# Kernel tuning notes

Measured on AMD Instinct MI355X. Metric: run time of the kernel, lower is better.

Reference implementation:

```python
import jax, jax.numpy as jnp
import numpy as np

B, S, W, T = 16, 32, 32, 64
H2 = 512   # num_hidden*2: decoder state / encoder state size
Hf = 256   # vocab_nn hidden (= num_hidden)
F = 128    # vectorizer.vector_size
A = 128    # attn_hidden (= num_hidden // 2)
V = 32000  # vocab size; distribution over V+1 (last slot = OOV / -1 index)


def setup_inputs() -> dict:
    key = jax.random.key(0)
    ks = jax.random.split(key, 24)
    p = lambda k, shp, s=0.05: (jax.random.normal(k, shp) * s).astype(jnp.float32)
    d = {}
    d["text_states"] = p(ks[0], (B, S, W, H2), 0.5)
    d["sentence_states"] = p(ks[1], (B, S, H2), 0.5)
    d["text_length"] = jnp.clip(jax.random.randint(ks[2], (B, S), 0, W), 1, W)
    d["state"] = p(ks[3], (B, 2, H2), 0.5)
    d["summary"] = jax.random.randint(ks[4], (B, T), 0, V)
    d["summary_length"] = jnp.clip(jax.random.randint(ks[5], (B,), 0, T), 2, T)
    d["emb"] = p(ks[6], (V + 1, F), 0.02)            # vectorizer embedding
    d["W_cc"] = p(ks[7], (F + H2, F)); d["b_cc"] = jnp.zeros((F,), jnp.float32)
    d["Wx"] = p(ks[8], (F, 4 * H2)); d["Wh"] = p(ks[9], (H2, 4 * H2))
    d["b_lstm"] = jnp.zeros((4 * H2,), jnp.float32)
    d["W_a"] = p(ks[10], (2 * H2 + 1, A)); d["b_a"] = jnp.zeros((A,), jnp.float32)
    d["v_a"] = p(ks[11], (A,))
    d["W_rc"] = p(ks[12], (2 * H2, H2)); d["b_rc"] = jnp.zeros((H2,), jnp.float32)
    d["W1"] = p(ks[13], (2 * H2, Hf)); d["b1"] = jnp.zeros((Hf,), jnp.float32)
    d["W2"] = p(ks[14], (Hf, V + 1)); d["b2"] = jnp.zeros((V + 1,), jnp.float32)
    return d


def reference(text_states, sentence_states, text_length, state, summary,
              summary_length, emb, W_cc, b_cc, Wx, Wh, b_lstm,
              W_a, b_a, v_a, W_rc, b_rc, W1, b1, W2, b2):
    SW = S * W
    ws = text_states.reshape(B, SW, H2)  # word states, flattened source positions
    ss = jnp.broadcast_to(sentence_states[:, :, None, :], (B, S, W, H2)).reshape(B, SW, H2)
    cat_states = jnp.concatenate([ws, ss], -1)               # (B,SW,4H)
    mask = (jnp.arange(W) < text_length[:, :, None]).reshape(B, SW)
    Wa_word, Wa_out, wa_cov = W_a[:H2], W_a[H2:2 * H2], W_a[2 * H2]
    ws_a = ws @ Wa_word + b_a                                # step-invariant, (B,SW,A)

    def step(carry, xs):
        st, coverage, ctx, loss = carry
        tok_t, tok_tp1, t = xs
        valid = ((summary_length - t - 1) > 0).astype(jnp.float32)
        # CombineContext + LSTM decoder cell
        x = jnp.concatenate([emb[tok_t], ctx], 1) @ W_cc + b_cc
        h, c = st[:, 0], st[:, 1]
        gi, gf, gg, go = jnp.split(x @ Wx + h @ Wh + b_lstm, 4, axis=1)
        c_new = jax.nn.sigmoid(gf) * c + jax.nn.sigmoid(gi) * jnp.tanh(gg)
        out = jax.nn.sigmoid(go) * jnp.tanh(c_new)           # (B,2H)
        # hierarchical attention with coverage feature (input dim 4H+1)
        scores = jnp.tanh(ws_a + (out @ Wa_out)[:, None, :]
                          + coverage[:, :, None] * wa_cov) @ v_a
        attn = jax.nn.softmax(jnp.where(mask, scores, -1e9), axis=1)
        ctx4 = jnp.einsum('bn,bnd->bd', attn, cat_states)    # (B,4H)
        ctx_new = ctx4 @ W_rc + b_rc                         # ReduceContextVector -> (B,2H)
        # vocabulary distribution
        hid = jax.nn.relu(jnp.concatenate([ctx_new, out], 1) @ W1 + b1)
        vocab = jax.nn.softmax(hid @ W2 + b2, axis=1)        # (B,V+1)
        tgt = jnp.where(tok_tp1 == -1, V, tok_tp1)           # map_input_indices_
        logp = jnp.log(jnp.take_along_axis(vocab, tgt[:, None], 1)[:, 0])
        covloss = jnp.minimum(coverage, attn).sum(1)
        loss = loss + valid * (-logp + covloss)              # gamma = 1
        # scatter-back semantics of timestep_wrapper: invalid rows zeroed
        attn_m = attn * valid[:, None]
        st_new = jnp.stack([out, c_new], 1) * valid[:, None, None]
        return (st_new, coverage + attn_m, ctx_new * valid[:, None], loss), None

    coverage0 = jnp.zeros((B, SW), jnp.float32)
    ctx0 = jnp.zeros((B, H2), jnp.float32)
    loss0 = jnp.zeros((B,), jnp.float32)
    xs = (summary[:, :-1].T, summary[:, 1:].T, jnp.arange(T - 1))
    (_, _, _, loss), _ = jax.lax.scan(step, (state, coverage0, ctx0, loss0), xs)
    return loss / (summary_length.astype(jnp.float32) - 1.0)
```

## Files before the change

### kernel.cpp

```cpp
#include <hip/hip_runtime.h>
#include <math.h>

#define B 16
#define S 32
#define T 64
#define H2 512
#define Hf 256
#define F 128
#define A 128
#define V 32000
#define SW 1024
#define NSTEP 63
#define VP1 32001
#define NBLK 256

__device__ __forceinline__ float frcp(float x){ return __builtin_amdgcn_rcpf(x); }
__device__ __forceinline__ float fsigm(float x){ return frcp(1.f + __expf(-x)); }
__device__ __forceinline__ float ftanh_(float x){
    float e = __expf(-2.f*fabsf(x));
    float t = (1.f - e)*frcp(1.f + e);
    return x >= 0.f ? t : -t;
}
__device__ __forceinline__ void ast(float* p, float v){
    __hip_atomic_store(p, v, __ATOMIC_RELAXED, __HIP_MEMORY_SCOPE_AGENT);
// ... 118 lines not shown
    }
}

__global__ __launch_bounds__(128) void k_wrcc(
    const float* __restrict__ W_rc, const float* __restrict__ W_cc, float* __restrict__ WRCC)
{
    __shared__ float wr[512];
    int d = blockIdx.x, f = threadIdx.x;
    for (int i = f; i < 512; i += 128) wr[i] = W_rc[(size_t)d*H2 + i];
    __syncthreads();
    float a = 0.f;
    for (int c = 0; c < H2; ++c) a += wr[c]*W_cc[(size_t)(F+c)*F + f];
    WRCC[(size_t)d*F + f] = a;
}

__global__ __launch_bounds__(128) void k_embx(
    const int* __restrict__ summary, const float* __restrict__ emb,
    const float* __restrict__ W_cc, const float* __restrict__ b_cc,
    float* __restrict__ embx)
{
    __shared__ float er[128];
    int t = blockIdx.x, b = blockIdx.y, f = threadIdx.x;
    int tok = summary[b*T + t];
    er[f] = emb[(size_t)tok*F + f];
    __syncthreads();
    float a = b_cc[f];
    for (int k = 0; k < F; ++k) a += er[k]*W_cc[(size_t)k*F + f];
    embx[((size_t)t*B + b)*F + f] = a;
}

__global__ __launch_bounds__(1024) void k_packw2(
    const float* __restrict__ W2, unsigned* __restrict__ W2h)
{
    size_t idx = (size_t)blockIdx.x*1024 + threadIdx.x;
    int rp = (int)(idx >> 15), v = (int)(idx & 32767);
    float lo = (v < VP1) ? W2[(size_t)(2*rp)*VP1 + v] : 0.f;
    float hi = (v < VP1) ? W2[(size_t)(2*rp+1)*VP1 + v] : 0.f;
    W2h[idx] = bfr(lo) | (bfr(hi) << 16);
}
__global__ __launch_bounds__(1024) void k_packws(
    const float* __restrict__ ws, unsigned* __restrict__ wsh)
{
    size_t idx = (size_t)blockIdx.x*1024 + threadIdx.x;
    int b = (int)(idx >> 18), r = (int)(idx & 262143);
    int np = r >> 9, d = r & 511;
    float lo = ws[((size_t)b*SW + 2*np)*H2 + d];
    float hi = ws[((size_t)b*SW + 2*np+1)*H2 + d];
    wsh[idx] = bfr(lo) | (bfr(hi) << 16);
}
__global__ __launch_bounds__(1024) void k_packwsa(
    const float* __restrict__ ws_aT, unsigned* __restrict__ ws_aTh)
{
    size_t idx = (size_t)blockIdx.x*1024 + threadIdx.x;
    int b = (int)(idx >> 16), r = (int)(idx & 65535);
    int ap = r >> 10, n = r & 1023;
    float lo = ws_aT[((size_t)b*A + 2*ap)*SW + n];
    float hi = ws_aT[((size_t)b*A + 2*ap+1)*SW + n];
    ws_aTh[idx] = bfr(lo) | (bfr(hi) << 16);
}
__global__ __launch_bounds__(1024) void k_packwg(
    const float* __restrict__ Wx, const float* __restrict__ Wh,
    unsigned* __restrict__ wgh)
{
    size_t idx = (size_t)blockIdx.x*1024 + threadIdx.x;
    int kp = (int)(idx >> 11), cg = (int)(idx & 2047);
    int k0 = 2*kp, k1 = 2*kp + 1;
    float lo = (k0 < F) ? Wx[(size_t)k0*2048 + cg] : Wh[(size_t)(k0-F)*2048 + cg];
    float hi = (k1 < F) ? Wx[(size_t)k1*2048 + cg] : Wh[(size_t)(k1-F)*2048 + cg];
    wgh[idx] = bfr(lo) | (bfr(hi) << 16);
}

__global__ __launch_bounds__(512, 2) void k_persist(
    const float* __restrict__ ss,
    const int* __restrict__ text_length, const int* __restrict__ summary,
    const int* __restrict__ sumlen, const float* __restrict__ state,
    const unsigned* __restrict__ wgh, const float* __restrict__ b_lstm,
    const float* __restrict__ W_a, const float* __restrict__ v_a,
    const float* __restrict__ W1, const float* __restrict__ b2,
    const unsigned* __restrict__ W2h, const unsigned* __restrict__ wsh,
    const unsigned* __restrict__ ws_aTh,
    const float* __restrict__ Wf, const float* __restrict__ bf,
    const float* __restrict__ WRCC, const float* __restrict__ bconst,
    const float* __restrict__ embx,
    float* xR, float* outR, float* hidR, float* scoresR, float* c4R,
    unsigned* wopartH, float* mpartR, float* spartR, float* m2R, float* s2R,
    float* tgtlogR, float* covlpR, float* d_out, unsigned* cnt)
{
    __shared__ unsigned W2L[16384];
    __shared__ unsigned wsaL[4096];
    __shared__ float BIG[15552];
    __shared__ float redS[576];
    __shared__ float red2[528];
    __shared__ float wo_l[128];
    __shared__ float wac_l[128], vas_l[128], b2_l[128];
    __shared__ float score_l[64], cov_l[64];
    __shared__ float c_l[128];
    __shared__ float gsum[528];
    __shared__ float asum_l[32];
    __shared__ float mred[136], sred[136], msc2[16];
    __shared__ float loss_l[16];
    __shared__ float misc[4];
    __shared__ int tl_l[32], sumlen_l[16], tgt_l[16];

    const int blk = blockIdx.x, tid = threadIdx.x;
    const int b_role = blk >> 4, sl = blk & 15;
    unsigned* arr = cnt;
    unsigned* rel = cnt + 8192;

    const int vl = tid & 127, rq = tid >> 7;
    const int dl = tid & 31, nq = tid >> 5;
    const int n3 = tid & 63, aq = tid >> 6;
    const int cc = tid & 31, kg = tid >> 5;

    unsigned wsr[32];
    #pragma unroll
    for (int j = 0; j < 32; ++j)
        wsr[j] = wsh[((size_t)b_role*512 + nq*32 + j)*512 + sl*32 + dl];
    unsigned wgr[20];
    if (blk < 64){
        const int CGg = (cc >> 3)*512 + blk*8 + (cc & 7);
        #pragma unroll
        for (int j = 0; j < 20; ++j)
            wgr[j] = wgh[(size_t)(kg*20 + j)*2048 + CGg];
    }
    #pragma unroll
    for (int q = 0; q < 32; ++q){
        int i = q*512 + tid;
        W2L[i] = W2h[(size_t)(i >> 7)*32768 + blk*128 + (i & 127)];
    }
    #pragma unroll
    for (int q = 0; q < 8; ++q){
        int i = q*512 + tid;
        wsaL[i] = ws_aTh[((size_t)(b_role*64 + (i >> 6)))*1024 + sl*64 + (i & 63)];
    }

    if (tid < 128){
        wac_l[tid] = W_a[(size_t)(2*H2)*A + tid];
        vas_l[tid] = v_a[tid];
        int v2 = blk*128 + tid;
        b2_l[tid] = (v2 < VP1) ? b2[v2] : 0.f;
    }
    if (tid < 32) tl_l[tid] = text_length[b_role*S + tid];
    if (tid < 16){ sumlen_l[tid] = sumlen[tid]; loss_l[tid] = 0.f; }
    if (tid < 64) cov_l[tid] = 0.f;
    if (blk < 64 && tid < 128){
        int b = tid >> 3, c = tid & 7;
        c_l[tid] = state[(size_t)b*2*H2 + H2 + blk*8 + c];
    }
    __syncthreads();

    unsigned gen = 0;
    for (int t = 0; t <= NSTEP; ++t){
        if (t >= 1){
            if (tid < 16) mred[tid] = mpartR[(size_t)(t-1)*256 + b_role*16 + tid];
            if (tid >= 16 && tid < 32) mred[tid] = spartR[(size_t)(t-1)*256 + b_role*16 + (tid-16)];
            __syncthreads();
            if (tid == 0){
                float M = -1e30f;
                for (int i = 0; i < 16; ++i) M = fmaxf(M, mred[i]);
                float Sv = 0.f;
                for (int i = 0; i < 16; ++i) Sv += mred[16+i]*__expf(mred[i]-M);
                misc[0] = M; misc[1] = frcp(Sv);
            }
            __syncthreads();
            if (tid < 64){
                float at = __expf(score_l[tid]-misc[0])*misc[1];
                float clp = fminf(cov_l[tid], at);
                float vm1 = (sumlen_l[b_role] - t > 0) ? 1.f : 0.f;
                cov_l[tid] += at*vm1;
                sred[tid] = clp;
            }
            __syncthreads();
            if (tid == 0){
                float s = 0.f;
                for (int i = 0; i < 64; ++i) s += sred[i];
                ast(&covlpR[(size_t)(t-1)*256 + b_role*16 + sl], s);
            }
            __syncthreads();
        }
        if (t < NSTEP && blk < 64){
            float* xh = BIG;
            float* outloc = BIG + 14336;
            float* waL = BIG + 14464;
            {
                int i2 = tid*2;
                waL[i2]   = W_a[(size_t)(H2 + blk*8 + (i2 >> 7))*A + (i2 & 127)];
                waL[i2+1] = W_a[(size_t)(H2 + blk*8 + ((i2+1) >> 7))*A + ((i2+1) & 127)];
            }
            const float* xb0 = xR + (size_t)t*B*F;
            const float* hb0 = outR + (size_t)(t > 0 ? t-1 : 0)*B*H2;
            #pragma unroll
            for (int q = 0; q < 20; ++q){
                int i = q*512 + tid;
                int b = i/640, k = i - b*640;
                float v;
                if (k < F) v = xb0[b*F + k];
                else if (t == 0) v = state[(size_t)b*2*H2 + (k - F)];
                else v = hb0[b*H2 + (k - F)] * ((sumlen_l[b] - t > 0) ? 1.f : 0.f);
                xh[i] = v;
            }
            __syncthreads();
            for (int b = 0; b < 16; ++b){
                const float* xb = &BIG[b*640 + kg*40];
                float s0 = 0.f, s1 = 0.f;
                #pragma unroll
                for (int j = 0; j < 20; ++j){
                    unsigned wu = wgr[j];
                    s0 = fmaf(xb[2*j],   blo(wu), s0);
                    s1 = fmaf(xb[2*j+1], bhi(wu), s1);
                }
                float p = s0 + s1;
                p += __shfl_xor(p, 32);
                if ((kg & 1) == 0)
                    BIG[10240 + (b*8 + (kg >> 1))*32 + cc] = p;
            }
            __syncthreads();
            {
                int b = tid >> 5, c2 = tid & 31;
                float s = 0.f;
                #pragma unroll
                for (int q = 0; q < 8; ++q) s += BIG[10240 + (b*8 + q)*32 + c2];
                gsum[b*33 + c2] = s;
            }
            __syncthreads();
            if (tid < 128){
                int b = tid >> 3, c = tid & 7, col = blk*8 + c;
                float gi = gsum[b*33 + c]      + b_lstm[col];
                float gf = gsum[b*33 + 8 + c]  + b_lstm[H2 + col];
                float gg = gsum[b*33 + 16 + c] + b_lstm[2*H2 + col];
                float go = gsum[b*33 + 24 + c] + b_lstm[3*H2 + col];
                float cold = c_l[tid];
                float cn = fsigm(gf)*cold + fsigm(gi)*ftanh_(gg);
                float o = fsigm(go)*ftanh_(cn);
                float valid = (sumlen_l[b] - t - 1 > 0) ? 1.f : 0.f;
                c_l[tid] = cn*valid;
                outloc[tid] = o;
                ast(&outR[(size_t)t*B*H2 + b*H2 + col], o);
            }
            __syncthreads();
            {
                int o2 = tid*2;
                int b = o2 >> 6, ap0 = o2 & 63;
                #pragma unroll
                for (int w = 0; w < 2; ++w){
                    int ap = ap0 + w, a0 = ap*2;
                    float acc0 = 0.f, acc1 = 0.f;
                    #pragma unroll
                    for (int j = 0; j < 8; ++j){
                        float ov = outloc[b*8 + j];
                        acc0 = fmaf(ov, waL[j*128 + a0],     acc0);
                        acc1 = fmaf(ov, waL[j*128 + a0 + 1], acc1);
                    }
                    astu(&wopartH[(size_t)t*65536 + blk*1024 + b*64 + ap],
                         bfr(acc0) | (bfr(acc1) << 16));
                }
            }
        }
        gen++; gbar(arr, rel, gen);

        if (t < NSTEP){
            {
                int ap = tid & 63, grp = tid >> 6;
                const unsigned* wp = wopartH + (size_t)t*65536 + (size_t)(grp*8)*1024
                                     + b_role*64 + ap;
                float lo = 0.f, hi = 0.f;
                #pragma unroll
                for (int q = 0; q < 8; ++q){
                    unsigned u = wp[(size_t)q*1024];
                    lo += blo(u); hi += bhi(u);
                }
                red2[ap*8 + grp] = lo;
                redS[ap*8 + grp] = hi;
            }
            __syncthreads();
            if (tid < 64){
                float lo = 0.f, hi = 0.f;
                #pragma unroll
                for (int q = 0; q < 8; ++q){ lo += red2[tid*8+q]; hi += redS[tid*8+q]; }
                wo_l[tid*2] = lo; wo_l[tid*2+1] = hi;
            }
            __syncthreads();
            {
                float cv = cov_l[n3];
                float acc = 0.f;
                #pragma unroll
                for (int i = 0; i < 8; ++i){
                    unsigned u = wsaL[(aq*8 + i)*64 + n3];
                    int a0 = aq*16 + 2*i;
                    acc = fmaf(ftanh_(blo(u) + wo_l[a0] + cv*wac_l[a0]), vas_l[a0], acc);
                    acc = fmaf(ftanh_(bhi(u) + wo_l[a0+1] + cv*wac_l[a0+1]), vas_l[a0+1], acc);
                }
                redS[aq*72 + n3] = acc;
            }
            __syncthreads();
            if (tid < 64){
                float s = 0.f;
                #pragma unroll
                for (int q = 0; q < 8; ++q) s += redS[q*72 + tid];
                int nn = sl*64 + tid;
                float sc = ((nn & 31) < tl_l[nn >> 5]) ? s : -1e9f;
                score_l[tid] = sc;
                ast(&scoresR[(size_t)t*B*SW + b_role*SW + nn], sc);
            }
            __syncthreads();
            if (tid == 0){
                float m = score_l[0];
                for (int i = 1; i < 64; ++i) m = fmaxf(m, score_l[i]);
                float s = 0.f;
                for (int i = 0; i < 64; ++i) s += __expf(score_l[i]-m);
                ast(&mpartR[(size_t)t*256 + b_role*16 + sl], m);
                ast(&spartR[(size_t)t*256 + b_role*16 + sl], s);
            }
        }
        gen++; gbar(arr, rel, gen);

        {
            float* SC = BIG;
            float* AT = BIG + 1024;
            float* redc = BIG + 2048;
            float* hidL = BIG + 2560;
            float* parts = BIG + 6784;
            float* logitl = BIG;
            if (t < NSTEP){
                #pragma unroll
                for (int q = 0; q < 2; ++q)
                    SC[q*512 + tid] = scoresR[(size_t)t*B*SW + b_role*SW + q*512 + tid];
                if (tid < 16) mred[tid] = mpartR[(size_t)t*256 + b_role*16 + tid];
                if (tid >= 16 && tid < 32) mred[tid] = spartR[(size_t)t*256 + b_role*16 + (tid-16)];
            }
            if (t >= 1){
                if (tid < 16){ int tok = summary[tid*T + t]; tgt_l[tid] = (tok == -1) ? V : tok; }
                #pragma unroll
                for (int q = 0; q < 8; ++q){
                    int idx = q*512 + tid;
                    int r = idx >> 4, b = idx & 15;
                    hidL[b*264 + r] = hidR[(size_t)(t-1)*B*Hf + idx];
                }
            }
            __syncthreads();
            if (t < NSTEP){
                if (tid == 0){
                    float M = -1e30f;
                    for (int i = 0; i < 16; ++i) M = fmaxf(M, mred[i]);
                    float Sv = 0.f;
                    for (int i = 0; i < 16; ++i) Sv += mred[16+i]*__expf(mred[i]-M);
                    misc[0] = M; misc[1] = frcp(Sv);
                }
            }
            __syncthreads();
            if (t < NSTEP){
                #pragma unroll
                for (int q = 0; q < 2; ++q){
                    int n = q*512 + tid;
                    AT[n] = __expf(SC[n]-misc[0])*misc[1];
                }
            }
            __syncthreads();
            if (t < NSTEP){
                if (tid < 32){
                    float s = 0.f;
                    #pragma unroll
                    for (int j = 0; j < 32; ++j) s += AT[tid*32 + ((j + tid) & 31)];
                    asum_l[tid] = s;
                }
                float acc0 = 0.f, acc1 = 0.f;
                const float2* at2 = (const float2*)&AT[nq*64];
                #pragma unroll
                for (int j = 0; j < 32; ++j){
                    unsigned u = wsr[j];
                    float2 av = at2[j];
                    acc0 = fmaf(av.x, blo(u), acc0);
                    acc1 = fmaf(av.y, bhi(u), acc1);
                }
                redc[nq*32 + dl] = acc0 + acc1;
            }
            if (t >= 1){
                unsigned wreg[32];
                #pragma unroll
                for (int i = 0; i < 32; ++i) wreg[i] = W2L[(rq*32 + i)*128 + vl];
                for (int b = 0; b < 16; ++b){
                    const float2* hb2 = (const float2*)&hidL[b*264 + rq*64];
                    float a0 = 0.f, a1 = 0.f;
                    #pragma unroll
                    for (int i = 0; i < 32; ++i){
                        unsigned u = wreg[i];
                        float2 h = hb2[i];
                        a0 = fmaf(h.x, blo(u), a0);
                        a1 = fmaf(h.y, bhi(u), a1);
                    }
                    parts[rq*2176 + vl*17 + b] = a0 + a1;
                }
            }
            __syncthreads();
            if (t < NSTEP){
                if (tid < 32){
                    float s = 0.f;
                    #pragma unroll
                    for (int q = 0; q < 16; ++q) s += redc[q*32 + tid];
                    ast(&c4R[(size_t)t*B*SW + b_role*SW + sl*32 + tid], s);
                } else if (tid < 64){
                    int d2 = tid - 32;
                    float s = 0.f;
                    const float* ssb = ss + ((size_t)(b_role*S))*H2 + sl*32 + d2;
                    #pragma unroll 4
                    for (int s2 = 0; s2 < 32; ++s2)
                        s = fmaf(asum_l[s2], ssb[(size_t)s2*H2], s);
                    ast(&c4R[(size_t)t*B*SW + b_role*SW + 512 + sl*32 + d2], s);
                }
            }
            __syncthreads();
            if (t >= 1){
                #pragma unroll
                for (int j = 0; j < 4; ++j){
                    int idx = tid*4 + j;
                    int vl2 = idx >> 4, bb = idx & 15;
                    float s = parts[0*2176 + vl2*17 + bb]
                            + parts[1*2176 + vl2*17 + bb]
                            + parts[2*2176 + vl2*17 + bb]
                            + parts[3*2176 + vl2*17 + bb];
                    int v2 = blk*128 + vl2;
                    float lg = (v2 < VP1) ? (s + b2_l[vl2]) : -1e30f;
                    if (v2 < VP1 && v2 == tgt_l[bb])
                        ast(&tgtlogR[(size_t)(t-1)*16 + bb], lg);
                    logitl[vl2*17 + bb] = lg;
                }
                __syncthreads();
                if (tid < 128){
                    int b2i = tid & 15, grp = tid >> 4;
                    float m = -1e30f;
                    #pragma unroll
                    for (int i = 0; i < 16; ++i) m = fmaxf(m, logitl[(grp*16+i)*17 + b2i]);
                    mred[grp*17 + b2i] = m;
                }
                __syncthreads();
                if (tid < 16){
                    float m = -1e30f;
                    #pragma unroll
                    for (int q = 0; q < 8; ++q) m = fmaxf(m, mred[q*17 + tid]);
                    msc2[tid] = m;
                }
                __syncthreads();
                if (tid < 128){
                    int b2i = tid & 15, grp = tid >> 4;
                    float Mb = msc2[b2i];
                    float s = 0.f;
                    #pragma unroll
                    for (int i = 0; i < 16; ++i) s += __expf(logitl[(grp*16+i)*17 + b2i] - Mb);
                    sred[grp*17 + b2i] = s;
                }
                __syncthreads();
                if (tid < 16){
                    float s = 0.f;
                    #pragma unroll
                    for (int q = 0; q < 8; ++q) s += sred[q*17 + tid];
                    ast(&m2R[(size_t)(t-1)*B*256 + tid*256 + blk], msc2[tid]);
                    ast(&s2R[(size_t)(t-1)*B*256 + tid*256 + blk], s);
                }
            }
        }
        gen++; gbar(arr, rel, gen);

        if (t < NSTEP && sl < 12){
            float* c4l = BIG;
            float* OL  = BIG + 1024;
            float* redd = BIG + 1536;
            #pragma unroll
            for (int q = 0; q < 2; ++q)
                c4l[q*512 + tid] = c4R[(size_t)t*B*SW + b_role*SW + q*512 + tid];
            if (tid < 512) OL[tid] = outR[(size_t)t*B*H2 + b_role*H2 + tid];
            __syncthreads();
            int cl = tid & 31, kq = tid >> 5;
            if (sl < 8){
                int col = sl*32 + cl;
                float acc = 0.f;
                const float* wp = Wf + (size_t)(kq*64)*Hf + col;
                #pragma unroll 4
                for (int i = 0; i < 64; ++i)
                    acc = fmaf(c4l[kq*64+i], wp[(size_t)i*Hf], acc);
                const float* w1p = W1 + (size_t)(H2 + kq*32)*Hf + col;
                #pragma unroll 4
                for (int i = 0; i < 32; ++i)
                    acc = fmaf(OL[kq*32+i], w1p[(size_t)i*Hf], acc);
                redd[kq*32 + cl] = acc;
                __syncthreads();
                if (tid < 32){
                    float z = 0.f;
                    #pragma unroll
                    for (int q = 0; q < 16; ++q) z += redd[q*32 + tid];
                    z += bf[sl*32 + tid];
                    ast(&hidR[(size_t)t*B*Hf + (sl*32 + tid)*16 + b_role], fmaxf(z, 0.f));
                }
            } else {
                int f = (sl-8)*32 + cl;
                float acc = 0.f;
                const float* wp = WRCC + (size_t)(kq*64)*F + f;
                #pragma unroll 4
                for (int i = 0; i < 64; ++i)
                    acc = fmaf(c4l[kq*64+i], wp[(size_t)i*F], acc);
                redd[kq*32 + cl] = acc;
                __syncthreads();
                if (tid < 32){
                    int f2 = (sl-8)*32 + tid;
                    float z = 0.f;
                    #pragma unroll
                    for (int q = 0; q < 16; ++q) z += redd[q*32 + tid];
                    float vld = (sumlen_l[b_role] - t - 1 > 0) ? 1.f : 0.f;
                    float xv = embx[((size_t)(t+1)*B + b_role)*F + f2] + vld*(z + bconst[f2]);
                    ast(&xR[(size_t)(t+1)*B*F + b_role*F + f2], xv);
                }
            }
        }
        if (t >= 1 && blk == 255 && tid < 256){
            int tf = t - 1;
            int bb = tid >> 4, g = tid & 15;
            float mv[16];
            float m = -1e30f;
            #pragma unroll
            for (int j = 0; j < 16; ++j){
                mv[j] = m2R[(size_t)tf*B*256 + bb*256 + g + j*16];
                m = fmaxf(m, mv[j]);
            }
            #pragma unroll
            for (int off = 1; off < 16; off <<= 1) m = fmaxf(m, __shfl_xor(m, off, 16));
            float s = 0.f;
            #pragma unroll
            for (int j = 0; j < 16; ++j)
                s += s2R[(size_t)tf*B*256 + bb*256 + g + j*16]*__expf(mv[j]-m);
            #pragma unroll
            for (int off = 1; off < 16; off <<= 1) s += __shfl_xor(s, off, 16);
            if (g == 0){
                float cl = 0.f;
                for (int q = 0; q < 16; ++q) cl += covlpR[(size_t)tf*256 + bb*16 + q];
                float tlg = tgtlogR[(size_t)tf*16 + bb];
                float logp = tlg - m - __logf(s);
                float vld = (sumlen_l[bb] - tf - 1 > 0) ? 1.f : 0.f;
                loss_l[bb] += vld*(-logp + cl);
                if (t == NSTEP) d_out[bb] = loss_l[bb] / ((float)sumlen_l[bb] - 1.f);
            }
        }
        if (t == NSTEP) break;
        gen++; gbar(arr, rel, gen);
    }
}

extern "C" void kernel_launch(void* const* d_in, const int* in_sizes, int n_in,
                              void* d_out, int out_size, void* d_ws, size_t ws_size,
                              hipStream_t stream) {
    const float* text_states = (const float*)d_in[0];
    const float* sent_states = (const float*)d_in[1];
    const int*   text_length = (const int*)d_in[2];
    const float* state       = (const float*)d_in[3];
    const int*   summary     = (const int*)d_in[4];
    const int*   sumlen      = (const int*)d_in[5];
    const float* emb    = (const float*)d_in[6];
    const float* W_cc   = (const float*)d_in[7];
    const float* b_cc   = (const float*)d_in[8];
    const float* Wx     = (const float*)d_in[9];
    const float* Wh     = (const float*)d_in[10];
    const float* b_lstm = (const float*)d_in[11];
    const float* W_a    = (const float*)d_in[12];
    const float* b_a    = (const float*)d_in[13];
    const float* v_a    = (const float*)d_in[14];
    const float* W_rc   = (const float*)d_in[15];
    const float* b_rc   = (const float*)d_in[16];
    const float* W1     = (const float*)d_in[17];
    const float* b1     = (const float*)d_in[18];
    const float* W2     = (const float*)d_in[19];
    const float* b2     = (const float*)d_in[20];
    float* out = (float*)d_out;

    float* p = (float*)d_ws;
    float* ws_aT   = p; p += (size_t)B*A*SW;
    float* Wf      = p; p += (size_t)1024*Hf;
    float* bfv     = p; p += Hf;
    float* WRCC    = p; p += (size_t)1024*F;
    float* bconst  = p; p += F;
    float* embx    = p; p += (size_t)T*B*F;
    float* xR      = p; p += (size_t)(NSTEP+1)*B*F;
    float* outR    = p; p += (size_t)(NSTEP+1)*B*H2;
    float* hidR    = p; p += (size_t)(NSTEP+1)*B*Hf;
    float* scoresR = p; p += (size_t)(NSTEP+1)*B*SW;
    float* c4R     = p; p += (size_t)(NSTEP+1)*B*SW;
    float* mpartR  = p; p += (size_t)(NSTEP+1)*256;
    float* spartR  = p; p += (size_t)(NSTEP+1)*256;
    float* m2R     = p; p += (size_t)(NSTEP+1)*B*256;
    float* s2R     = p; p += (size_t)(NSTEP+1)*B*256;
    float* tgtlogR = p; p += (size_t)(NSTEP+1)*16;
    float* covlpR  = p; p += (size_t)(NSTEP+1)*256;
    unsigned* cnt  = (unsigned*)p; p += 8704;
    unsigned* W2h    = (unsigned*)p; p += (size_t)128*32768;
    unsigned* wsh    = (unsigned*)p; p += (size_t)16*512*512;
    unsigned* ws_aTh = (unsigned*)p; p += (size_t)16*64*1024;
    unsigned* wgh    = (unsigned*)p; p += (size_t)320*2048;
    unsigned* wopartH= (unsigned*)p; p += (size_t)NSTEP*65536;

    k_init0<<<17, 256, 0, stream>>>(emb, W_cc, b_cc, summary, xR, cnt);
    k_wsa<<<dim3(B, 64), 256, 0, stream>>>(text_states, W_a, b_a, ws_aT);
    k_wf<<<257, 256, 0, stream>>>(W_rc, b_rc, W1, b1, W_cc, Wf, bfv, bconst);
    k_wrcc<<<1024, 128, 0, stream>>>(W_rc, W_cc, WRCC);
    k_embx<<<dim3(T, B), 128, 0, stream>>>(summary, emb, W_cc, b_cc, embx);
    k_packw2<<<4096, 1024, 0, stream>>>(W2, W2h);
    k_packws<<<4096, 1024, 0, stream>>>(text_states, wsh);
    k_packwsa<<<1024, 1024, 0, stream>>>(ws_aT, ws_aTh);
    k_packwg<<<640, 1024, 0, stream>>>(Wx, Wh, wgh);
    k_persist<<<NBLK, 512, 0, stream>>>(
        sent_states, text_length, summary, sumlen, state,
        wgh, b_lstm, W_a, v_a, W1, b2,
        W2h, wsh, ws_aTh, Wf, bfv, WRCC, bconst, embx,
        xR, outR, hidR, scoresR, c4R, wopartH, mpartR, spartR, m2R, s2R,
        tgtlogR, covlpR, out, cnt);
}
```

Before: 4.489 ms.

## Use unnormalized attention softmax to remove a grid barrier per decode step

The attention softmax is restructured to use a fixed offset (exp of unnormalized scores), so each block publishes packed partial exp values and partial sums instead of a max/sum pair needing a separate global reduction phase. The context-vector reduction is merged with the hidden/vocab phase and the word-state weights are re-laid out so each thread owns a column, which removes scoresR/c4R round trips and at least one grid-wide barrier per step. The final loss for the last step moves after the loop. Skipping the max subtraction risks overflow if scores grow large; the bounded tanh-based scores make this plausible but it is a numerical assumption.

```diff
diff --git a/kernel.cpp b/kernel.cpp
--- a/kernel.cpp
+++ b/kernel.cpp
@@ -224,9 +224,10 @@
     const float* __restrict__ Wf, const float* __restrict__ bf,
     const float* __restrict__ WRCC, const float* __restrict__ bconst,
     const float* __restrict__ embx,
-    float* xR, float* outR, float* hidR, float* scoresR, float* c4R,
-    unsigned* wopartH, float* mpartR, float* spartR, float* m2R, float* s2R,
-    float* tgtlogR, float* covlpR, float* d_out, unsigned* cnt)
+    float* xR, float* outR, float* hidR,
+    unsigned* wopartH, unsigned* PpkR, float* ZpartR, float* asumR,
+    float* m2R, float* s2R, float* tgtlogR, float* covlpR,
+    float* d_out, unsigned* cnt)
 {
     __shared__ unsigned W2L[16384];
     __shared__ unsigned wsaL[4096];
@@ -235,13 +236,13 @@
     __shared__ float red2[528];
     __shared__ float wo_l[128];
     __shared__ float wac_l[128], vas_l[128], b2_l[128];
-    __shared__ float score_l[64], cov_l[64];
+    __shared__ float expU_l[64], cov_l[64];
     __shared__ float c_l[128];
     __shared__ float gsum[528];
     __shared__ float asum_l[32];
     __shared__ float mred[136], sred[136], msc2[16];
     __shared__ float loss_l[16];
-    __shared__ float misc[4];
+    __shared__ float Zsh;
     __shared__ int tl_l[32], sumlen_l[16], tgt_l[16];
 
     const int blk = blockIdx.x, tid = threadIdx.x;
@@ -250,14 +251,13 @@
     unsigned* rel = cnt + 8192;
 
     const int vl = tid & 127, rq = tid >> 7;
-    const int dl = tid & 31, nq = tid >> 5;
     const int n3 = tid & 63, aq = tid >> 6;
     const int cc = tid & 31, kg = tid >> 5;
 
-    unsigned wsr[32];
+    unsigned wsrN[32];
     #pragma unroll
     for (int j = 0; j < 32; ++j)
-        wsr[j] = wsh[((size_t)b_role*512 + nq*32 + j)*512 + sl*32 + dl];
+        wsrN[j] = wsh[((size_t)b_role*512 + sl*32 + j)*512 + tid];
     unsigned wgr[20];
     if (blk < 64){
         const int CGg = (cc >> 3)*512 + blk*8 + (cc & 7);
@@ -294,366 +294,21 @@
     unsigned gen = 0;
     for (int t = 0; t <= NSTEP; ++t){
         if (t >= 1){
-            if (tid < 16) mred[tid] = mpartR[(size_t)(t-1)*256 + b_role*16 + tid];
-            if (tid >= 16 && tid < 32) mred[tid] = spartR[(size_t)(t-1)*256 + b_role*16 + (tid-16)];
-            __syncthreads();
-            if (tid == 0){
-                float M = -1e30f;
-                for (int i = 0; i < 16; ++i) M = fmaxf(M, mred[i]);
-                float Sv = 0.f;
-                for (int i = 0; i < 16; ++i) Sv += mred[16+i]*__expf(mred[i]-M);
-                misc[0] = M; misc[1] = frcp(Sv);
-            }
-            __syncthreads();
+            float invZ = frcp(Zsh);
             if (tid < 64){
-                float at = __expf(score_l[tid]-misc[0])*misc[1];
+                float at = expU_l[tid]*invZ;
                 float clp = fminf(cov_l[tid], at);
                 float vm1 = (sumlen_l[b_role] - t > 0) ? 1.f : 0.f;
                 cov_l[tid] += at*vm1;
-                sred[tid] = clp;
-            }
-            __syncthreads();
-            if (tid == 0){
-                float s = 0.f;
-                for (int i = 0; i < 64; ++i) s += sred[i];
-                ast(&covlpR[(size_t)(t-1)*256 + b_role*16 + sl], s);
-            }
-            __syncthreads();
-        }
-        if (t < NSTEP && blk < 64){
-            float* xh = BIG;
-            float* outloc = BIG + 14336;
-            float* waL = BIG + 14464;
-            {
-                int i2 = tid*2;
-                waL[i2]   = W_a[(size_t)(H2 + blk*8 + (i2 >> 7))*A + (i2 & 127)];
-                waL[i2+1] = W_a[(size_t)(H2 + blk*8 + ((i2+1) >> 7))*A + ((i2+1) & 127)];
-            }
-            const float* xb0 = xR + (size_t)t*B*F;
-            const float* hb0 = outR + (size_t)(t > 0 ? t-1 : 0)*B*H2;
-            #pragma unroll
-            for (int q = 0; q < 20; ++q){
-                int i = q*512 + tid;
-                int b = i/640, k = i - b*640;
-                float v;
-                if (k < F) v = xb0[b*F + k];
-                else if (t == 0) v = state[(size_t)b*2*H2 + (k - F)];
-                else v = hb0[b*H2 + (k - F)] * ((sumlen_l[b] - t > 0) ? 1.f : 0.f);
-                xh[i] = v;
-            }
-            __syncthreads();
-            for (int b = 0; b < 16; ++b){
-                const float* xb = &BIG[b*640 + kg*40];
-                float s0 = 0.f, s1 = 0.f;
-                #pragma unroll
-                for (int j = 0; j < 20; ++j){
-                    unsigned wu = wgr[j];
-                    s0 = fmaf(xb[2*j],   blo(wu), s0);
-                    s1 = fmaf(xb[2*j+1], bhi(wu), s1);
-                }
-                float p = s0 + s1;
-                p += __shfl_xor(p, 32);
-                if ((kg & 1) == 0)
-                    BIG[10240 + (b*8 + (kg >> 1))*32 + cc] = p;
-            }
-            __syncthreads();
-            {
-                int b = tid >> 5, c2 = tid & 31;
-                float s = 0.f;
-                #pragma unroll
-                for (int q = 0; q < 8; ++q) s += BIG[10240 + (b*8 + q)*32 + c2];
-                gsum[b*33 + c2] = s;
-            }
-            __syncthreads();
-            if (tid < 128){
-                int b = tid >> 3, c = tid & 7, col = blk*8 + c;
-                float gi = gsum[b*33 + c]      + b_lstm[col];
-                float gf = gsum[b*33 + 8 + c]  + b_lstm[H2 + col];
-                float gg = gsum[b*33 + 16 + c] + b_lstm[2*H2 + col];
-                float go = gsum[b*33 + 24 + c] + b_lstm[3*H2 + col];
-                float cold = c_l[tid];
-                float cn = fsigm(gf)*cold + fsigm(gi)*ftanh_(gg);
-                float o = fsigm(go)*ftanh_(cn);
-                float valid = (sumlen_l[b] - t - 1 > 0) ? 1.f : 0.f;
-                c_l[tid] = cn*valid;
-                outloc[tid] = o;
-                ast(&outR[(size_t)t*B*H2 + b*H2 + col], o);
-            }
-            __syncthreads();
-            {
-                int o2 = tid*2;
-                int b = o2 >> 6, ap0 = o2 & 63;
-                #pragma unroll
-                for (int w = 0; w < 2; ++w){
-                    int ap = ap0 + w, a0 = ap*2;
-                    float acc0 = 0.f, acc1 = 0.f;
-                    #pragma unroll
-                    for (int j = 0; j < 8; ++j){
-                        float ov = outloc[b*8 + j];
-                        acc0 = fmaf(ov, waL[j*128 + a0],     acc0);
-                        acc1 = fmaf(ov, waL[j*128 + a0 + 1], acc1);
-                    }
-                    astu(&wopartH[(size_t)t*65536 + blk*1024 + b*64 + ap],
-                         bfr(acc0) | (bfr(acc1) << 16));
-                }
-            }
-        }
-        gen++; gbar(arr, rel, gen);
-
-        if (t < NSTEP){
-            {
-                int ap = tid & 63, grp = tid >> 6;
-                const unsigned* wp = wopartH + (size_t)t*65536 + (size_t)(grp*8)*1024
-                                     + b_role*64 + ap;
-                float lo = 0.f, hi = 0.f;
-                #pragma unroll
-                for (int q = 0; q < 8; ++q){
-                    unsigned u = wp[(size_t)q*1024];
-                    lo += blo(u); hi += bhi(u);
-                }
-                red2[ap*8 + grp] = lo;
-                redS[ap*8 + grp] = hi;
-            }
-            __syncthreads();
-            if (tid < 64){
-                float lo = 0.f, hi = 0.f;
-                #pragma unroll
-                for (int q = 0; q < 8; ++q){ lo += red2[tid*8+q]; hi += redS[tid*8+q]; }
-                wo_l[tid*2] = lo; wo_l[tid*2+1] = hi;
-            }
-            __syncthreads();
-            {
-                float cv = cov_l[n3];
-                float acc = 0.f;
-                #pragma unroll
-                for (int i = 0; i < 8; ++i){
-                    unsigned u = wsaL[(aq*8 + i)*64 + n3];
-                    int a0 = aq*16 + 2*i;
-                    acc = fmaf(ftanh_(blo(u) + wo_l[a0] + cv*wac_l[a0]), vas_l[a0], acc);
-                    acc = fmaf(ftanh_(bhi(u) + wo_l[a0+1] + cv*wac_l[a0+1]), vas_l[a0+1], acc);
-                }
-                redS[aq*72 + n3] = acc;
-            }
-            __syncthreads();
-            if (tid < 64){
-                float s = 0.f;
-                #pragma unroll
-                for (int q = 0; q < 8; ++q) s += redS[q*72 + tid];
-                int nn = sl*64 + tid;
-                float sc = ((nn & 31) < tl_l[nn >> 5]) ? s : -1e9f;
-                score_l[tid] = sc;
-                ast(&scoresR[(size_t)t*B*SW + b_role*SW + nn], sc);
-            }
-            __syncthreads();
-            if (tid == 0){
-                float m = score_l[0];
-                for (int i = 1; i < 64; ++i) m = fmaxf(m, score_l[i]);
-                float s = 0.f;
-                for (int i = 0; i < 64; ++i) s += __expf(score_l[i]-m);
-                ast(&mpartR[(size_t)t*256 + b_role*16 + sl], m);
-                ast(&spartR[(size_t)t*256 + b_role*16 + sl], s);
-            }
-        }
-        gen++; gbar(arr, rel, gen);
-
-        {
-            float* SC = BIG;
-            float* AT = BIG + 1024;
-            float* redc = BIG + 2048;
-            float* hidL = BIG + 2560;
-            float* parts = BIG + 6784;
-            float* logitl = BIG;
-            if (t < NSTEP){
-                #pragma unroll
-                for (int q = 0; q < 2; ++q)
-                    SC[q*512 + tid] = scoresR[(size_t)t*B*SW + b_role*SW + q*512 + tid];
-                if (tid < 16) mred[tid] = mpartR[(size_t)t*256 + b_role*16 + tid];
-                if (tid >= 16 && tid < 32) mred[tid] = spartR[(size_t)t*256 + b_role*16 + (tid-16)];
-            }
-            if (t >= 1){
-                if (tid < 16){ int tok = summary[tid*T + t]; tgt_l[tid] = (tok == -1) ? V : tok; }
-                #pragma unroll
-                for (int q = 0; q < 8; ++q){
-                    int idx = q*512 + tid;
-                    int r = idx >> 4, b = idx & 15;
-                    hidL[b*264 + r] = hidR[(size_t)(t-1)*B*Hf + idx];
-                }
-            }
-            __syncthreads();
-            if (t < NSTEP){
-                if (tid == 0){
-                    float M = -1e30f;
-                    for (int i = 0; i < 16; ++i) M = fmaxf(M, mred[i]);
-                    float Sv = 0.f;
-                    for (int i = 0; i < 16; ++i) Sv += mred[16+i]*__expf(mred[i]-M);
-                    misc[0] = M; misc[1] = frcp(Sv);
-                }
-            }
-            __syncthreads();
-            if (t < NSTEP){
-                #pragma unroll
-                for (int q = 0; q < 2; ++q){
-                    int n = q*512 + tid;
-                    AT[n] = __expf(SC[n]-misc[0])*misc[1];
-                }
-            }
-            __syncthreads();
-            if (t < NSTEP){
-                if (tid < 32){
-                    float s = 0.f;
-                    #pragma unroll
-                    for (int j = 0; j < 32; ++j) s += AT[tid*32 + ((j + tid) & 31)];
-                    asum_l[tid] = s;
-                }
-                float acc0 = 0.f, acc1 = 0.f;
-                const float2* at2 = (const float2*)&AT[nq*64];
-                #pragma unroll
-                for (int j = 0; j < 32; ++j){
-                    unsigned u = wsr[j];
-                    float2 av = at2[j];
-                    acc0 = fmaf(av.x, blo(u), acc0);
-                    acc1 = fmaf(av.y, bhi(u), acc1);
-                }
-                redc[nq*32 + dl] = acc0 + acc1;
-            }
-            if (t >= 1){
-                unsigned wreg[32];
-                #pragma unroll
-                for (int i = 0; i < 32; ++i) wreg[i] = W2L[(rq*32 + i)*128 + vl];
-                for (int b = 0; b < 16; ++b){
-                    const float2* hb2 = (const float2*)&hidL[b*264 + rq*64];
-                    float a0 = 0.f, a1 = 0.f;
-                    #pragma unroll
-                    for (int i = 0; i < 32; ++i){
-                        unsigned u = wreg[i];
-                        float2 h = hb2[i];
-                        a0 = fmaf(h.x, blo(u), a0);
-                        a1 = fmaf(h.y, bhi(u), a1);
-                    }
-                    parts[rq*2176 + vl*17 + b] = a0 + a1;
-                }
-            }
-            __syncthreads();
-            if (t < NSTEP){
-                if (tid < 32){
-                    float s = 0.f;
-                    #pragma unroll
-                    for (int q = 0; q < 16; ++q) s += redc[q*32 + tid];
-                    ast(&c4R[(size_t)t*B*SW + b_role*SW + sl*32 + tid], s);
-                } else if (tid < 64){
-                    int d2 = tid - 32;
-                    float s = 0.f;
-                    const float* ssb = ss + ((size_t)(b_role*S))*H2 + sl*32 + d2;
-                    #pragma unroll 4
-                    for (int s2 = 0; s2 < 32; ++s2)
-                        s = fmaf(asum_l[s2], ssb[(size_t)s2*H2], s);
-                    ast(&c4R[(size_t)t*B*SW + b_role*SW + 512 + sl*32 + d2], s);
-                }
-            }
-            __syncthreads();
-            if (t >= 1){
-                #pragma unroll
-                for (int j = 0; j < 4; ++j){
-                    int idx = tid*4 + j;
-                    int vl2 = idx >> 4, bb = idx & 15;
-                    float s = parts[0*2176 + vl2*17 + bb]
-                            + parts[1*2176 + vl2*17 + bb]
-                            + parts[2*2176 + vl2*17 + bb]
-                            + parts[3*2176 + vl2*17 + bb];
-                    int v2 = blk*128 + vl2;
-                    float lg = (v2 < VP1) ? (s + b2_l[vl2]) : -1e30f;
-                    if (v2 < VP1 && v2 == tgt_l[bb])
-                        ast(&tgtlogR[(size_t)(t-1)*16 + bb], lg);
-                    logitl[vl2*17 + bb] = lg;
-                }
-                __syncthreads();
-                if (tid < 128){
-                    int b2i = tid & 15, grp = tid >> 4;
-                    float m = -1e30f;
-                    #pragma unroll
-                    for (int i = 0; i < 16; ++i) m = fmaxf(m, logitl[(grp*16+i)*17 + b2i]);
-                    mred[grp*17 + b2i] = m;
-                }
-                __syncthreads();
-                if (tid < 16){
-                    float m = -1e30f;
-                    #pragma unroll
-                    for (int q = 0; q < 8; ++q) m = fmaxf(m, mred[q*17 + tid]);
-                    msc2[tid] = m;
-                }
-                __syncthreads();
-                if (tid < 128){
-                    int b2i = tid & 15, grp = tid >> 4;
-                    float Mb = msc2[b2i];
-                    float s = 0.f;
-                    #pragma unroll
-                    for (int i = 0; i < 16; ++i) s += __expf(logitl[(grp*16+i)*17 + b2i] - Mb);
-                    sred[grp*17 + b2i] = s;
-                }
-                __syncthreads();
-                if (tid < 16){
-                    float s = 0.f;
-                    #pragma unroll
-                    for (int q = 0; q < 8; ++q) s += sred[q*17 + tid];
-                    ast(&m2R[(size_t)(t-1)*B*256 + tid*256 + blk], msc2[tid]);
-                    ast(&s2R[(size_t)(t-1)*B*256 + tid*256 + blk], s);
-                }
-            }
-        }
-        gen++; gbar(arr, rel, gen);
-
-        if (t < NSTEP && sl < 12){
-            float* c4l = BIG;
-            float* OL  = BIG + 1024;
-            float* redd = BIG + 1536;
-            #pragma unroll
-            for (int q = 0; q < 2; ++q)
-                c4l[q*512 + tid] = c4R[(size_t)t*B*SW + b_role*SW + q*512 + tid];
-            if (tid < 512) OL[tid] = outR[(size_t)t*B*H2 + b_role*H2 + tid];
-            __syncthreads();
-            int cl = tid & 31, kq = tid >> 5;
-            if (sl < 8){
-                int col = sl*32 + cl;
-                float acc = 0.f;
-                const float* wp = Wf + (size_t)(kq*64)*Hf + col;
-                #pragma unroll 4
-                for (int i = 0; i < 64; ++i)
-                    acc = fmaf(c4l[kq*64+i], wp[(size_t)i*Hf], acc);
-                const float* w1p = W1 + (size_t)(H2 + kq*32)*Hf + col;
-                #pragma unroll 4
-                for (int i = 0; i < 32; ++i)
-                    acc = fmaf(OL[kq*32+i], w1p[(size_t)i*Hf], acc);
-                redd[kq*32 + cl] = acc;
-                __syncthreads();
-                if (tid < 32){
-                    float z = 0.f;
-                    #pragma unroll
-                    for (int q = 0; q < 16; ++q) z += redd[q*32 + tid];
-                    z += bf[sl*32 + tid];
-                    ast(&hidR[(size_t)t*B*Hf + (sl*32 + tid)*16 + b_role], fmaxf(z, 0.f));
-                }
-            } else {
-                int f = (sl-8)*32 + cl;
-                float acc = 0.f;
-                const float* wp = WRCC + (size_t)(kq*64)*F + f;
-                #pragma unroll 4
-                for (int i = 0; i < 64; ++i)
-                    acc = fmaf(c4l[kq*64+i], wp[(size_t)i*F], acc);
-                redd[kq*32 + cl] = acc;
-                __syncthreads();
-                if (tid < 32){
-                    int f2 = (sl-8)*32 + tid;
-                    float z = 0.f;
-                    #pragma unroll
-                    for (int q = 0; q < 16; ++q) z += redd[q*32 + tid];
-                    float vld = (sumlen_l[b_role] - t - 1 > 0) ? 1.f : 0.f;
-                    float xv = embx[((size_t)(t+1)*B + b_role)*F + f2] + vld*(z + bconst[f2]);
-                    ast(&xR[(size_t)(t+1)*B*F + b_role*F + f2], xv);
-                }
-            }
-        }
-        if (t >= 1 && blk == 255 && tid < 256){
-            int tf = t - 1;
+                float s = clp;
+                s += __shfl_xor(s, 1);  s += __shfl_xor(s, 2);
+                s += __shfl_xor(s, 4);  s += __shfl_xor(s, 8);
+                s += __shfl_xor(s, 16); s += __shfl_xor(s, 32);
+                if (tid == 0) ast(&covlpR[(size_t)(t-1)*256 + b_role*16 + sl], s);
+            }
+        }
+        if (t >= 2 && blk == 255 && tid < 256){
+            int tf = t - 2;
             int bb = tid >> 4, g = tid & 15;
             float mv[16];
             float m = -1e30f;
@@ -677,11 +332,348 @@
                 float logp = tlg - m - __logf(s);
                 float vld = (sumlen_l[bb] - tf - 1 > 0) ? 1.f : 0.f;
                 loss_l[bb] += vld*(-logp + cl);
-                if (t == NSTEP) d_out[bb] = loss_l[bb] / ((float)sumlen_l[bb] - 1.f);
-            }
-        }
-        if (t == NSTEP) break;
+            }
+        }
+        if (t < NSTEP && blk < 64){
+            float* xh = BIG;
+            float* outloc = BIG + 14336;
+            float* waL = BIG + 14464;
+            {
+                int i2 = tid*2;
+                waL[i2]   = W_a[(size_t)(H2 + blk*8 + (i2 >> 7))*A + (i2 & 127)];
+                waL[i2+1] = W_a[(size_t)(H2 + blk*8 + ((i2+1) >> 7))*A + ((i2+1) & 127)];
+            }
+            const float* xb0 = xR + (size_t)t*B*F;
+            const float* hb0 = outR + (size_t)(t > 0 ? t-1 : 0)*B*H2;
+            #pragma unroll
+            for (int q = 0; q < 20; ++q){
+                int i = q*512 + tid;
+                int b = i/640, k = i - b*640;
+                float v;
+                if (k < F) v = xb0[b*F + k];
+                else if (t == 0) v = state[(size_t)b*2*H2 + (k - F)];
+                else v = hb0[b*H2 + (k - F)] * ((sumlen_l[b] - t > 0) ? 1.f : 0.f);
+                xh[i] = v;
+            }
+            __syncthreads();
+            for (int b = 0; b < 16; ++b){
+                const float* xb = &BIG[b*640 + kg*40];
+                float s0 = 0.f, s1 = 0.f;
+                #pragma unroll
+                for (int j = 0; j < 20; ++j){
+                    unsigned wu = wgr[j];
+                    s0 = fmaf(xb[2*j],   blo(wu), s0);
+                    s1 = fmaf(xb[2*j+1], bhi(wu), s1);
+                }
+                float p = s0 + s1;
+                p += __shfl_xor(p, 32);
+                if ((kg & 1) == 0)
+                    BIG[10240 + (b*8 + (kg >> 1))*32 + cc] = p;
+            }
+            __syncthreads();
+            {
+                int b = tid >> 5, c2 = tid & 31;
+                float s = 0.f;
+                #pragma unroll
+                for (int q = 0; q < 8; ++q) s += BIG[10240 + (b*8 + q)*32 + c2];
+                gsum[b*33 + c2] = s;
+            }
+            __syncthreads();
+            if (tid < 128){
+                int b = tid >> 3, c = tid & 7, col = blk*8 + c;
+                float gi = gsum[b*33 + c]      + b_lstm[col];
+                float gf = gsum[b*33 + 8 + c]  + b_lstm[H2 + col];
+                float gg = gsum[b*33 + 16 + c] + b_lstm[2*H2 + col];
+                float go = gsum[b*33 + 24 + c] + b_lstm[3*H2 + col];
+                float cold = c_l[tid];
+                float cn = fsigm(gf)*cold + fsigm(gi)*ftanh_(gg);
+                float o = fsigm(go)*ftanh_(cn);
+                float valid = (sumlen_l[b] - t - 1 > 0) ? 1.f : 0.f;
+                c_l[tid] = cn*valid;
+                outloc[tid] = o;
+                ast(&outR[(size_t)t*B*H2 + b*H2 + col], o);
+            }
+            __syncthreads();
+            {
+                int o2 = tid*2;
+                int b = o2 >> 6, ap0 = o2 & 63;
+                #pragma unroll
+                for (int w = 0; w < 2; ++w){
+                    int ap = ap0 + w, a0 = ap*2;
+                    float acc0 = 0.f, acc1 = 0.f;
+                    #pragma unroll
+                    for (int j = 0; j < 8; ++j){
+                        float ov = outloc[b*8 + j];
+                        acc0 = fmaf(ov, waL[j*128 + a0],     acc0);
+                        acc1 = fmaf(ov, waL[j*128 + a0 + 1], acc1);
+                    }
+                    astu(&wopartH[(size_t)t*65536 + blk*1024 + b*64 + ap],
+                         bfr(acc0) | (bfr(acc1) << 16));
+                }
+            }
+        }
         gen++; gbar(arr, rel, gen);
+
+        if (t < NSTEP){
+            {
+                int ap = tid & 63, grp = tid >> 6;
+                const unsigned* wp = wopartH + (size_t)t*65536 + (size_t)(grp*8)*1024
+                                     + b_role*64 + ap;
+                float lo = 0.f, hi = 0.f;
+                #pragma unroll
+                for (int q = 0; q < 8; ++q){
+                    unsigned u = wp[(size_t)q*1024];
+                    lo += blo(u); hi += bhi(u);
+                }
+                red2[ap*8 + grp] = lo;
+                redS[ap*8 + grp] = hi;
+            }
+            __syncthreads();
+            if (tid < 64){
+                float lo = 0.f, hi = 0.f;
+                #pragma unroll
+                for (int q = 0; q < 8; ++q){ lo += red2[tid*8+q]; hi += redS[tid*8+q]; }
+                wo_l[tid*2] = lo; wo_l[tid*2+1] = hi;
+            }
+            __syncthreads();
+            {
+                float cv = cov_l[n3];
+                float acc = 0.f;
+                #pragma unroll
+                for (int i = 0; i < 8; ++i){
+                    unsigned u = wsaL[(aq*8 + i)*64 + n3];
+                    int a0 = aq*16 + 2*i;
+                    acc = fmaf(ftanh_(blo(u) + wo_l[a0] + cv*wac_l[a0]), vas_l[a0], acc);
+                    acc = fmaf(ftanh_(bhi(u) + wo_l[a0+1] + cv*wac_l[a0+1]), vas_l[a0+1], acc);
+                }
+                redS[aq*72 + n3] = acc;
+            }
+            __syncthreads();
+            if (tid < 64){
+                float s = 0.f;
+                #pragma unroll
+                for (int q = 0; q < 8; ++q) s += redS[q*72 + tid];
+                int nn = sl*64 + tid;
+                float sc = ((nn & 31) < tl_l[nn >> 5]) ? s : -1e9f;
+                float e = __expf(sc);
+                expU_l[tid] = e;
+                float h = e;
+                h += __shfl_xor(h, 1);  h += __shfl_xor(h, 2);
+                h += __shfl_xor(h, 4);  h += __shfl_xor(h, 8);
+                h += __shfl_xor(h, 16);
+                float other = __shfl_xor(h, 32);
+                if (tid == 0){
+                    ast(&asumR[(size_t)t*512 + b_role*32 + sl*2 + 0], h);
+                    ast(&asumR[(size_t)t*512 + b_role*32 + sl*2 + 1], other);
+                    ast(&ZpartR[(size_t)t*256 + b_role*16 + sl], h + other);
+                }
+            }
+            __syncthreads();
+            {
+                float p = 0.f;
+                #pragma unroll
+                for (int j = 0; j < 32; ++j){
+                    unsigned u = wsrN[j];
+                    p = fmaf(expU_l[2*j],   blo(u), p);
+                    p = fmaf(expU_l[2*j+1], bhi(u), p);
+                }
+                BIG[tid] = p;
+            }
+            __syncthreads();
+            if (tid < 256)
+                astu(&PpkR[((size_t)t*256 + blk)*256 + tid],
+                     bfr(BIG[2*tid]) | (bfr(BIG[2*tid+1]) << 16));
+        }
+        gen++; gbar(arr, rel, gen);
+
+        {
+            float* c4l  = BIG;
+            float* OL   = BIG + 1024;
+            float* redd = BIG + 1536;
+            float* hidL = BIG + 2560;
+            float* parts = BIG + 6784;
+            float* logitl = parts;
+            if (t < NSTEP){
+                if (tid < 16) mred[tid] = ZpartR[(size_t)t*256 + b_role*16 + tid];
+                if (tid >= 32 && tid < 64) asum_l[tid-32] = asumR[(size_t)t*512 + b_role*32 + (tid-32)];
+                OL[tid] = outR[(size_t)t*B*H2 + b_role*H2 + tid];
+                if (tid < 256){
+                    float lo = 0.f, hi = 0.f;
+                    const unsigned* pp = PpkR + ((size_t)t*256 + b_role*16)*256 + tid;
+                    #pragma unroll
+                    for (int q = 0; q < 16; ++q){
+                        unsigned u = pp[(size_t)q*256];
+                        lo += blo(u); hi += bhi(u);
+                    }
+                    c4l[2*tid] = lo; c4l[2*tid+1] = hi;
+                }
+            }
+            if (t >= 1){
+                if (tid < 16){ int tok = summary[tid*T + t]; tgt_l[tid] = (tok == -1) ? V : tok; }
+                #pragma unroll
+                for (int q = 0; q < 8; ++q){
+                    int idx = q*512 + tid;
+                    int r = idx >> 4, b = idx & 15;
+                    hidL[b*264 + r] = hidR[(size_t)(t-1)*B*Hf + idx];
+                }
+            }
+            __syncthreads();
+            if (t < NSTEP && tid == 0){
+                float z = 0.f;
+                for (int i = 0; i < 16; ++i) z += mred[i];
+                Zsh = z;
+            }
+            __syncthreads();
+            if (t < NSTEP){
+                float invZ = frcp(Zsh);
+                float sent = 0.f;
+                const float* ssb = ss + (size_t)(b_role*S)*H2 + tid;
+                #pragma unroll 4
+                for (int s2 = 0; s2 < 32; ++s2)
+                    sent = fmaf(asum_l[s2], ssb[(size_t)s2*H2], sent);
+                float w = c4l[tid]*invZ;
+                c4l[tid] = w;
+                c4l[512 + tid] = sent*invZ;
+            }
+            __syncthreads();
+            if (t >= 1){
+                unsigned wreg[32];
+                #pragma unroll
+                for (int i = 0; i < 32; ++i) wreg[i] = W2L[(rq*32 + i)*128 + vl];
+                for (int b = 0; b < 16; ++b){
+                    const float2* hb2 = (const float2*)&hidL[b*264 + rq*64];
+                    float a0 = 0.f, a1 = 0.f;
+                    #pragma unroll
+                    for (int i = 0; i < 32; ++i){
+                        unsigned u = wreg[i];
+                        float2 h = hb2[i];
+                        a0 = fmaf(h.x, blo(u), a0);
+                        a1 = fmaf(h.y, bhi(u), a1);
+                    }
+                    parts[rq*2176 + vl*17 + b] = a0 + a1;
+                }
+            }
+            if (t < NSTEP && sl < 12){
+                int cl = tid & 31, kq = tid >> 5;
+                if (sl < 8){
+                    int col = sl*32 + cl;
+                    float acc = 0.f;
+                    const float* wp = Wf + (size_t)(kq*64)*Hf + col;
+                    #pragma unroll 4
+                    for (int i = 0; i < 64; ++i)
+                        acc = fmaf(c4l[kq*64+i], wp[(size_t)i*Hf], acc);
+                    const float* w1p = W1 + (size_t)(H2 + kq*32)*Hf + col;
+                    #pragma unroll 4
+                    for (int i = 0; i < 32; ++i)
+                        acc = fmaf(OL[kq*32+i], w1p[(size_t)i*Hf], acc);
+                    redd[kq*32 + cl] = acc;
+                } else {
+                    int f = (sl-8)*32 + cl;
+                    float acc = 0.f;
+                    const float* wp = WRCC + (size_t)(kq*64)*F + f;
+                    #pragma unroll 4
+                    for (int i = 0; i < 64; ++i)
+                        acc = fmaf(c4l[kq*64+i], wp[(size_t)i*F], acc);
+                    redd[kq*32 + cl] = acc;
+                }
+            }
+            __syncthreads();
+            if (t < NSTEP && sl < 12 && tid < 32){
+                if (sl < 8){
+                    float z = 0.f;
+                    #pragma unroll
+                    for (int q = 0; q < 16; ++q) z += redd[q*32 + tid];
+                    z += bf[sl*32 + tid];
+                    ast(&hidR[(size_t)t*B*Hf + (sl*32 + tid)*16 + b_role], fmaxf(z, 0.f));
+                } else {
+                    int f2 = (sl-8)*32 + tid;
+                    float z = 0.f;
+                    #pragma unroll
+                    for (int q = 0; q < 16; ++q) z += redd[q*32 + tid];
+                    float vld = (sumlen_l[b_role] - t - 1 > 0) ? 1.f : 0.f;
+                    float xv = embx[((size_t)(t+1)*B + b_role)*F + f2] + vld*(z + bconst[f2]);
+                    ast(&xR[(size_t)(t+1)*B*F + b_role*F + f2], xv);
+                }
+            }
+            if (t >= 1){
+                #pragma unroll
+                for (int j = 0; j < 4; ++j){
+                    int idx = tid*4 + j;
+                    int vl2 = idx >> 4, bb = idx & 15;
+                    float s = parts[0*2176 + vl2*17 + bb]
+                            + parts[1*2176 + vl2*17 + bb]
+                            + parts[2*2176 + vl2*17 + bb]
+                            + parts[3*2176 + vl2*17 + bb];
+                    int v2 = blk*128 + vl2;
+                    float lg = (v2 < VP1) ? (s + b2_l[vl2]) : -1e30f;
+                    if (v2 < VP1 && v2 == tgt_l[bb])
+                        ast(&tgtlogR[(size_t)(t-1)*16 + bb], lg);
+                    logitl[vl2*17 + bb] = lg;
+                }
+                __syncthreads();
+                if (tid < 128){
+                    int b2i = tid & 15, grp = tid >> 4;
+                    float m = -1e30f;
+                    #pragma unroll
+                    for (int i = 0; i < 16; ++i) m = fmaxf(m, logitl[(grp*16+i)*17 + b2i]);
+                    mred[grp*17 + b2i] = m;
+                }
+                __syncthreads();
+                if (tid < 16){
+                    float m = -1e30f;
+                    #pragma unroll
+                    for (int q = 0; q < 8; ++q) m = fmaxf(m, mred[q*17 + tid]);
+                    msc2[tid] = m;
+                }
+                __syncthreads();
+                if (tid < 128){
+                    int b2i = tid & 15, grp = tid >> 4;
+                    float Mb = msc2[b2i];
+                    float s = 0.f;
+                    #pragma unroll
+                    for (int i = 0; i < 16; ++i) s += __expf(logitl[(grp*16+i)*17 + b2i] - Mb);
+                    sred[grp*17 + b2i] = s;
+                }
+                __syncthreads();
+                if (tid < 16){
+                    float s = 0.f;
+                    #pragma unroll
+                    for (int q = 0; q < 8; ++q) s += sred[q*17 + tid];
+                    ast(&m2R[(size_t)(t-1)*B*256 + tid*256 + blk], msc2[tid]);
+                    ast(&s2R[(size_t)(t-1)*B*256 + tid*256 + blk], s);
+                }
+            }
+        }
+        gen++; gbar(arr, rel, gen);
+    }
+
+    if (blk == 255 && tid < 256){
+        int tf = NSTEP - 1;
+        int bb = tid >> 4, g = tid & 15;
+        float mv[16];
+        float m = -1e30f;
+        #pragma unroll
+        for (int j = 0; j < 16; ++j){
+            mv[j] = m2R[(size_t)tf*B*256 + bb*256 + g + j*16];
+            m = fmaxf(m, mv[j]);
+        }
+        #pragma unroll
+        for (int off = 1; off < 16; off <<= 1) m = fmaxf(m, __shfl_xor(m, off, 16));
+        float s = 0.f;
+        #pragma unroll
+        for (int j = 0; j < 16; ++j)
+            s += s2R[(size_t)tf*B*256 + bb*256 + g + j*16]*__expf(mv[j]-m);
+        #pragma unroll
+        for (int off = 1; off < 16; off <<= 1) s += __shfl_xor(s, off, 16);
+        if (g == 0){
+            float cl = 0.f;
+            for (int q = 0; q < 16; ++q) cl += covlpR[(size_t)tf*256 + bb*16 + q];
+            float tlg = tgtlogR[(size_t)tf*16 + bb];
+            float logp = tlg - m - __logf(s);
+            float vld = (sumlen_l[bb] - tf - 1 > 0) ? 1.f : 0.f;
+            loss_l[bb] += vld*(-logp + cl);
+            d_out[bb] = loss_l[bb] / ((float)sumlen_l[bb] - 1.f);
+        }
     }
 }
 
@@ -721,10 +713,8 @@
     float* xR      = p; p += (size_t)(NSTEP+1)*B*F;
     float* outR    = p; p += (size_t)(NSTEP+1)*B*H2;
     float* hidR    = p; p += (size_t)(NSTEP+1)*B*Hf;
-    float* scoresR = p; p += (size_t)(NSTEP+1)*B*SW;
-    float* c4R     = p; p += (size_t)(NSTEP+1)*B*SW;
-    float* mpartR  = p; p += (size_t)(NSTEP+1)*256;
-    float* spartR  = p; p += (size_t)(NSTEP+1)*256;
+    float* ZpartR  = p; p += (size_t)(NSTEP+1)*256;
+    float* asumR   = p; p += (size_t)(NSTEP+1)*512;
     float* m2R     = p; p += (size_t)(NSTEP+1)*B*256;
     float* s2R     = p; p += (size_t)(NSTEP+1)*B*256;
     float* tgtlogR = p; p += (size_t)(NSTEP+1)*16;
@@ -735,6 +725,7 @@
     unsigned* ws_aTh = (unsigned*)p; p += (size_t)16*64*1024;
     unsigned* wgh    = (unsigned*)p; p += (size_t)320*2048;
     unsigned* wopartH= (unsigned*)p; p += (size_t)NSTEP*65536;
+    unsigned* PpkR   = (unsigned*)p; p += (size_t)NSTEP*256*256;
 
     k_init0<<<17, 256, 0, stream>>>(emb, W_cc, b_cc, summary, xR, cnt);
     k_wsa<<<dim3(B, 64), 256, 0, stream>>>(text_states, W_a, b_a, ws_aT);
@@ -749,6 +740,6 @@
         sent_states, text_length, summary, sumlen, state,
         wgh, b_lstm, W_a, v_a, W1, b2,
         W2h, wsh, ws_aTh, Wf, bfv, WRCC, bconst, embx,
-        xR, outR, hidR, scoresR, c4R, wopartH, mpartR, spartR, m2R, s2R,
-        tgtlogR, covlpR, out, cnt);
-}
+        xR, outR, hidR, wopartH, PpkR, ZpartR, asumR,
+        m2R, s2R, tgtlogR, covlpR, out, cnt);
+}
```

Result: faster. 4.112 ms (-8.4%).
